# Optimization experiments

Hardware: AMD Instinct MI355X
Metric: run time of the kernel (lower is better)

## Reference

```python
import jax, jax.numpy as jnp
import numpy as np

B, G, N, D = 8, 16, 256, 768
E, S, SEQ = 1536, 128, 512
EPS = 1e-05


def rope_gn(x):
    # x: [b, g, n, h, s]; positions run over flattened (g, n), matching rope(x, dim=[1,2])
    g, n, half = x.shape[1], x.shape[2], x.shape[-1] // 2
    position = jnp.arange(g * n, dtype=jnp.float32).reshape(g, n)[:, :, None]  # [g,n,1]
    inv_freq = 10000.0 ** (jnp.arange(half, dtype=jnp.float32) / half)
    sinusoid = position[..., None] * inv_freq  # [g,n,1,half]
    sin, cos = jnp.sin(sinusoid), jnp.cos(sinusoid)
    x1, x2 = jnp.split(x, 2, axis=-1)
    return jnp.concatenate([x1 * cos - x2 * sin, x2 * cos + x1 * sin], axis=-1)


def rel_pos_bias(w, seq_len):
    # Toeplitz construction (seq_len <= 512 branch). w: [2*seq_len-1] -> [1, seq_len, seq_len]
    t = jnp.pad(w, (0, seq_len))                  # [3*seq_len-1]
    t = jnp.tile(t, seq_len)[:-seq_len]           # [seq_len*(3*seq_len-2)]
    t = t.reshape(seq_len, 3 * seq_len - 2)
    r = seq_len - 1                                # (2*seq_len-1)//2
    return t[:, r:-r][None]                        # [1, seq_len, seq_len]


def setup_inputs():
    key = jax.random.key(0)
    ks = jax.random.split(key, 8)
    inputs = jax.random.normal(ks[0], (B, G, N, D), dtype=jnp.float32)
    seg = jax.random.randint(ks[1], (B, G * N), 0, 4)
    segment_ids = jnp.sort(seg, axis=-1).reshape(B, G, N)
    params = {
        'ln_w': jnp.ones((D,), jnp.float32),
        'ln_b': jnp.zeros((D,), jnp.float32),
        'W1': jax.random.normal(ks[2], (D, 2 * E + S), jnp.float32) * 0.02,
        'b1': jnp.zeros((2 * E + S,), jnp.float32),
        'gamma': jax.random.uniform(ks[3], (4, S), jnp.float32),
        'beta': jax.random.uniform(ks[4], (4, S), jnp.float32),
        'W2': jax.random.normal(ks[5], (E, D), jnp.float32) * 0.02,
        'b2': jnp.zeros((D,), jnp.float32),
        'w_rel': jax.random.uniform(ks[6], (2 * SEQ - 1,), jnp.float32),
    }
    return dict(inputs=inputs, segment_ids=segment_ids, **params)


def reference(inputs, segment_ids, ln_w, ln_b, W1, b1, gamma, beta, W2, b2, w_rel):
    b, g, n, d = inputs.shape
    shortcut = inputs
    # LayerNorm
    mu = inputs.mean(-1, keepdims=True)
    var = ((inputs - mu) ** 2).mean(-1, keepdims=True)
    x = (inputs - mu) * jax.lax.rsqrt(var + EPS) * ln_w + ln_b
    # dense1 + silu, split into u, v, z
    uv = jax.nn.silu(x @ W1 + b1)
    u, v, z = uv[..., :E], uv[..., E:2 * E], uv[..., 2 * E:]
    # per-head affine gating + rope
    z = z[..., None, :] * gamma + beta            # [b,g,n,4,s]
    z = rope_gn(z)
    quad_q, quad_k, lin_q, lin_k = (z[..., i, :] for i in range(4))
    # non-causal global linear attention
    kv = jnp.einsum('bgcs,bgce->bse', lin_k, v)
    lin_v = jnp.einsum('bgcs,bse->bgce', lin_q, kv)
    lin_kv = jnp.einsum('bgnk,bgne->bgke', lin_k, lin_v) / n
    # segment mask over chunks
    mn = segment_ids.min(-1)
    mx = segment_ids.max(-1)
    mask = ((mn[:, :, None] <= mx[:, None, :]) & (mx[:, :, None] >= mn[:, None, :])).astype(inputs.dtype)
    mask = mask / mask.sum(-1, keepdims=True)
    lin_kv = jnp.einsum('bhke,bgh->bgke', lin_kv, mask)
    linear = jnp.einsum('bgnk,bgke->bgne', lin_q, lin_kv)
    # quadratic relu^2 attention with relative position bias
    qk = jnp.einsum('bgnk,bgmk->bgnm', quad_q, quad_k)
    bias = rel_pos_bias(w_rel, SEQ)[:, :n, :n]    # [1,n,n] broadcasts to [b,g,n,n]
    kernel = jnp.square(jax.nn.relu(qk / n + bias))
    quadratic = jnp.einsum('bgnm,bgme->bgne', kernel, v)
    out = (u * (quadratic + linear)) @ W2 + b2 + shortcut
    return out
```

## Files before the change

kernel.cpp:

```cpp
#include <hip/hip_runtime.h>
#include <math.h>

typedef __bf16 bf16;
typedef __bf16 bf16x8 __attribute__((ext_vector_type(8)));
typedef __bf16 bf16x4 __attribute__((ext_vector_type(4)));
typedef float  f32x4  __attribute__((ext_vector_type(4)));

#define D_   768
#define E_   1536
#define S_   128
#define TT_  32768
#define B_   8

#define OFF_W1T   0UL
#define OFF_W2T   4915200UL
#define OFF_TAB   7274496UL
#define OFF_XN    9375744UL
#define OFF_KER   OFF_XN
#define OFF_QQ    (OFF_XN + 16777216UL)
#define OFF_QK    (OFF_XN + 25165824UL)
#define OFF_LQ    (OFF_XN + 33554432UL)
#define OFF_U     59707392UL
#define OFF_Z     160370688UL
#define OFF_LK    168759296UL
#define OFF_LQT   177147904UL
#define OFF_LKT   185536512UL
#define OFF_MASK  193925120UL
#define OFF_INVF  193933312UL

__device__ __forceinline__ void gl_lds16(const bf16* g, bf16* l) {
  __builtin_amdgcn_global_load_lds(
      (const __attribute__((address_space(1))) unsigned int*)g,
      (__attribute__((address_space(3))) unsigned int*)l, 16, 0, 0);
}


#define STG(GB, LD, KT, DSTH) do {                                        \
  const int cg_ = (lane & 7) ^ ((lane >> 3) & 7);                         \
  const int rg_ = wave * 16 + ((lane >> 3) << 1) + (cg_ >> 2);            \
  gl_lds16((GB) + (long)rg_ * (LD) + (KT) * 32 + (cg_ & 3) * 8,           \
           (DSTH) + wave * 512);                                          \
} while (0)

template <class Epi, bool SWZ>
__global__ __launch_bounds__(512, 2) void gemm8p(
    const bf16* __restrict__ A, const bf16* __restrict__ B,
    int lda, int ldb, int K, Epi epi)
{
  __shared__ bf16 smem[4][4][4096];

  int bx = blockIdx.x, by = blockIdx.y;
  if constexpr (SWZ) {
    const int nbx = gridDim.x, nby = gridDim.y, nwg = nbx * nby;
    int bid = by * nbx + bx;
    const int q = nwg >> 3, r = nwg & 7;
    const int xcd = bid & 7, lid = bid >> 3;
    bid = (xcd < r ? xcd * (q + 1) : r * (q + 1) + (xcd - r) * q) + lid;
    const int gm = 8;
    const int pig = gm * nby;
    const int grp = bid / pig;
    const int fm = grp * gm;
    const int szm = min(nbx - fm, gm);
    const int loc = bid - grp * pig;
    bx = fm + loc % szm;
    by = loc / szm;
  }

  const int tid  = threadIdx.x;
  const int lane = tid & 63, wave = tid >> 6;
  const int wr = wave >> 2, wc = wave & 3;
  const int lrow = lane & 15, quad = lane >> 4;
  const int rb16 = (wc & 1) * 4;
  const int lbase = (lrow >> 1) * 128 +
                    (((((lrow & 1) << 2) | quad) ^ ((lrow >> 1) & 7)) * 16);

  const bf16* gA0 = A + (long)(bx * 256)       * lda;
  const bf16* gA1 = A + (long)(bx * 256 + 128) * lda;
  const bf16* gB0 = B + (long)(by * 256)       * ldb;
  const bf16* gB1 = B + (long)(by * 256 + 128) * ldb;

  f32x4 acc[8][4] = {};
  bf16x8 a0[4], a1[4], bfrag[4];

  const int NT = K >> 5;

#pragma unroll
  for (int t = 0; t < 3; ++t) {
    STG(gA0, lda, t, &smem[t][0][0]);
    STG(gA1, lda, t, &smem[t][1][0]);
    STG(gB0, ldb, t, &smem[t][2][0]);
    STG(gB1, ldb, t, &smem[t][3][0]);
  }
  asm volatile("s_waitcnt vmcnt(8)" ::: "memory");
  __builtin_amdgcn_s_barrier();
  __builtin_amdgcn_sched_barrier(0);

  for (int t = 0; t < NT; ++t) {
    const int st = t & 3, sp = (t + 3) & 3;
    const bf16* aBuf = &smem[st][wr][0];
    const bf16* bBuf = &smem[st][2 + (wc >> 1)][0];

#pragma unroll
    for (int mi = 0; mi < 4; ++mi)
      a0[mi] = *(const bf16x8*)((const char*)aBuf + mi * 1024 + lbase);
#pragma unroll
    for (int k = 0; k < 4; ++k)
      bfrag[k] = *(const bf16x8*)((const char*)bBuf + (rb16 + k) * 1024 + lbase);
#pragma unroll
    for (int mi = 0; mi < 4; ++mi)
      a1[mi] = *(const bf16x8*)((const char*)aBuf + (4 + mi) * 1024 + lbase);
    if (t + 3 < NT) {
      STG(gA0, lda, t + 3, &smem[sp][0][0]);
      STG(gB0, ldb, t + 3, &smem[sp][2][0]);
      STG(gA1, lda, t + 3, &smem[sp][1][0]);
      STG(gB1, ldb, t + 3, &smem[sp][3][0]);
    }

    __builtin_amdgcn_s_setprio(1);
#pragma unroll
    for (int mi = 0; mi < 4; ++mi)
#pragma unroll
      for (int n4 = 0; n4 < 4; ++n4)
        acc[mi][n4] = __builtin_amdgcn_mfma_f32_16x16x32_bf16(
            a0[mi], bfrag[n4], acc[mi][n4], 0, 0, 0);
#pragma unroll
    for (int mi = 0; mi < 4; ++mi)
#pragma unroll
      for (int n4 = 0; n4 < 4; ++n4)
        acc[4 + mi][n4] = __builtin_amdgcn_mfma_f32_16x16x32_bf16(
            a1[mi], bfrag[n4], acc[4 + mi][n4], 0, 0, 0);
    __builtin_amdgcn_s_setprio(0);

    __builtin_amdgcn_sched_barrier(0);
    if (t + 3 < NT)      asm volatile("s_waitcnt vmcnt(8)" ::: "memory");
    else if (t + 2 < NT) asm volatile("s_waitcnt vmcnt(4)" ::: "memory");
    else if (t + 1 < NT) asm volatile("s_waitcnt vmcnt(0)" ::: "memory");
    if (t + 1 < NT) {
      __builtin_amdgcn_s_barrier();
      __builtin_amdgcn_sched_barrier(0);
    }
  }

  const int rowbase = bx * 256 + wr * 128 + quad * 4;
  const int colbase = by * 256 + wc * 64 + lrow;
#pragma unroll
  for (int mi = 0; mi < 8; mi++)
#pragma unroll
    for (int ni = 0; ni < 4; ni++)
      epi(rowbase + mi * 16, colbase + ni * 16, 0, 0, acc[mi][ni]);
}

#define BM 128
#define BN 128
#define BK 32

template <class Epi, bool DUAL, bool SWZ = false>
__global__ __launch_bounds__(256) void gemm_bt(
    const bf16* __restrict__ A, const bf16* __restrict__ B,
    int lda, int ldb, int K,
    long sAb, long sAg, long sBb, long sBg,
    const bf16* __restrict__ A2, const bf16* __restrict__ B2,
    int lda2, int ldb2, int K2,
    long sA2b, long sA2g, long sB2b, long sB2g,
    int gdiv, Epi epi)
{
  __shared__ bf16 As[BM * BK];
  __shared__ bf16 Bs[BN * BK];
  const int z = blockIdx.z;
  const int bb = z / gdiv, gg = z % gdiv;

  int bx = blockIdx.x, by = blockIdx.y;
  if constexpr (SWZ) {
    const int nbx = gridDim.x, nby = gridDim.y, nwg = nbx * nby;
    int bid = by * nbx + bx;
    const int q = nwg >> 3, r = nwg & 7;
    const int xcd = bid & 7, lid = bid >> 3;
    bid = (xcd < r ? xcd * (q + 1) : r * (q + 1) + (xcd - r) * q) + lid;
    const int gm = 8;
    const int pig = gm * nby;
    const int grp = bid / pig;
    const int fm = grp * gm;
    const int szm = min(nbx - fm, gm);
    const int loc = bid - grp * pig;
    bx = fm + loc % szm;
    by = loc / szm;
  }

  const int tid  = threadIdx.x;
  const int lane = tid & 63, wave = tid >> 6;
  const int wm = (wave >> 1) * 64, wn = (wave & 1) * 64;
  const int lrow = lane & 15, quad = lane >> 4;
  const int srow = wave * 16 + (lane >> 2);
  const int scol = (lane & 3) * 8;
  bf16* ldsA0 = As + wave * 512;
  bf16* ldsA1 = As + (wave + 4) * 512;
  bf16* ldsB0 = Bs + wave * 512;
  bf16* ldsB1 = Bs + (wave + 4) * 512;

  f32x4 acc[4][4] = {};

  auto kloop = [&](const bf16* __restrict__ Ab, const bf16* __restrict__ Bb,
                   int lda_, int ldb_, int K_) {
    for (int k0 = 0; k0 < K_; k0 += BK) {
      __syncthreads();
      gl_lds16(Ab + (long)srow * lda_ + k0 + scol,        ldsA0);
      gl_lds16(Ab + (long)(srow + 64) * lda_ + k0 + scol, ldsA1);
      gl_lds16(Bb + (long)srow * ldb_ + k0 + scol,        ldsB0);
      gl_lds16(Bb + (long)(srow + 64) * ldb_ + k0 + scol, ldsB1);
      __syncthreads();
      bf16x8 af[4], bfr[4];
#pragma unroll
      for (int i = 0; i < 4; i++) af[i]  = *(const bf16x8*)&As[(wm + i * 16 + lrow) * BK + quad * 8];
#pragma unroll
      for (int i = 0; i < 4; i++) bfr[i] = *(const bf16x8*)&Bs[(wn + i * 16 + lrow) * BK + quad * 8];
#pragma unroll
      for (int mi = 0; mi < 4; mi++)
#pragma unroll
        for (int ni = 0; ni < 4; ni++)
          acc[mi][ni] = __builtin_amdgcn_mfma_f32_16x16x32_bf16(af[mi], bfr[ni], acc[mi][ni], 0, 0, 0);
    }
  };

  kloop(A + (long)bb * sAb + (long)gg * sAg + (long)bx * BM * lda,
        B + (long)bb * sBb + (long)gg * sBg + (long)by * BN * ldb, lda, ldb, K);
  if constexpr (DUAL)
    kloop(A2 + (long)bb * sA2b + (long)gg * sA2g + (long)bx * BM * lda2,
          B2 + (long)bb * sB2b + (long)gg * sB2g + (long)by * BN * ldb2, lda2, ldb2, K2);

  const int rowbase = bx * BM + wm + quad * 4;
  const int colbase = by * BN + wn + lrow;
#pragma unroll
  for (int mi = 0; mi < 4; mi++)
#pragma unroll
    for (int ni = 0; ni < 4; ni++)
      epi(rowbase + mi * 16, colbase + ni * 16, bb, gg, acc[mi][ni]);
}

struct EpiGemm1 {
  const float* b1; bf16* u; bf16* vT; bf16* z;
  __device__ void operator()(int row0, int col, int, int, f32x4 a) const {
    float s[4];
    const float bias = b1[col];
#pragma unroll
    for (int j = 0; j < 4; j++) {
      float x = a[j] + bias;
      float e = __expf(-x);
      s[j] = __fdividef(x, 1.f + e);
    }
    if (col < E_) {
#pragma unroll
      for (int j = 0; j < 4; j++) u[(long)(row0 + j) * E_ + col] = (bf16)s[j];
    } else if (col < 2 * E_) {
      const int e = col - E_, b = row0 >> 12, t = row0 & 4095;
      bf16x4 o;
#pragma unroll
      for (int j = 0; j < 4; j++) o[j] = (bf16)s[j];
      *(bf16x4*)&vT[((long)(b * E_ + e)) * 4096 + t] = o;
    } else {
      const int sc = col - 2 * E_;
#pragma unroll
      for (int j = 0; j < 4; j++) z[(long)(row0 + j) * S_ + sc] = (bf16)s[j];
    }
  }
};
struct EpiZ {
  const float* b1; bf16* z;
  __device__ void operator()(int row0, int col, int, int, f32x4 a) const {
    const float bias = b1[2 * E_ + col];
#pragma unroll
    for (int j = 0; j < 4; j++) {
      float x = a[j] + bias;
      float e = __expf(-x);
      z[(long)(row0 + j) * S_ + col] = (bf16)__fdividef(x, 1.f + e);
    }
  }
};
struct EpiF32 {
  float* C; long sCb, sCg; int ldc;
  __device__ void operator()(int row0, int col, int bb, int gg, f32x4 a) const {
#pragma unroll
    for (int j = 0; j < 4; j++)
      C[(long)bb * sCb + (long)gg * sCg + (long)(row0 + j) * ldc + col] = a[j];
  }
};
struct EpiBf16 {
  bf16* C; long sCb, sCg; int ldc;
  __device__ void operator()(int row0, int col, int bb, int gg, f32x4 a) const {
#pragma unroll
    for (int j = 0; j < 4; j++)
      C[(long)bb * sCb + (long)gg * sCg + (long)(row0 + j) * ldc + col] = (bf16)a[j];
  }
};
struct EpiKer {
  bf16* C; const float* wrel;
  __device__ void operator()(int row0, int col, int bb, int, f32x4 a) const {
#pragma unroll
    for (int j = 0; j < 4; j++) {
      float v = a[j] * (1.f / 256.f) + wrel[511 + col - (row0 + j)];
      v = fmaxf(v, 0.f);
      C[(long)bb * 65536 + (long)(row0 + j) * 256 + col] = (bf16)(v * v);
    }
  }
};
struct EpiCombine {
  bf16* u;
  __device__ void operator()(int row0, int col, int bb, int gg, f32x4 a) const {
#pragma unroll
    for (int j = 0; j < 4; j++) {
      long idx = ((long)((bb * 16 + gg) * 256 + row0 + j)) * E_ + col;
      u[idx] = (bf16)((float)u[idx] * a[j]);
    }
  }
};
struct EpiFinal {
  float* out; const float* b2; const float* x0;
  __device__ void operator()(int row0, int col, int, int, f32x4 a) const {
#pragma unroll
    for (int j = 0; j < 4; j++) {
      long idx = (long)(row0 + j) * D_ + col;
      out[idx] = a[j] + b2[col] + x0[idx];
    }
  }
};

__global__ __launch_bounds__(256) void ln_kernel(
    const float* __restrict__ x, const float* __restrict__ w,
    const float* __restrict__ b, bf16* __restrict__ xn)
{
  const long t = blockIdx.x;
  const float* row = x + t * D_;
  const int tid = threadIdx.x;
  float v0 = row[tid], v1 = row[tid + 256], v2 = row[tid + 512];
  float s = v0 + v1 + v2;
  float sq = v0 * v0 + v1 * v1 + v2 * v2;
#pragma unroll
  for (int off = 32; off; off >>= 1) {
    s  += __shfl_down(s, off, 64);
    sq += __shfl_down(sq, off, 64);
  }
  __shared__ float red[2][4];
  const int wave = tid >> 6, lane = tid & 63;
  if (lane == 0) { red[0][wave] = s; red[1][wave] = sq; }
  __syncthreads();
  s  = red[0][0] + red[0][1] + red[0][2] + red[0][3];
  sq = red[1][0] + red[1][1] + red[1][2] + red[1][3];
  const float mean = s * (1.f / 768.f);
  const float var  = sq * (1.f / 768.f) - mean * mean;
  const float rs   = rsqrtf(var + 1e-5f);
  xn[t * D_ + tid]       = (bf16)((v0 - mean) * rs * w[tid] + b[tid]);
  xn[t * D_ + tid + 256] = (bf16)((v1 - mean) * rs * w[tid + 256] + b[tid + 256]);
  xn[t * D_ + tid + 512] = (bf16)((v2 - mean) * rs * w[tid + 512] + b[tid + 512]);
}

template <class TI>
__global__ __launch_bounds__(256) void transpose_cast(
    const TI* __restrict__ in, bf16* __restrict__ out,
    int R, int C, long sInB, long sOutB)
{
  __shared__ float tile[64][65];
  const TI* ib = in  + (long)blockIdx.z * sInB;
  bf16*     ob = out + (long)blockIdx.z * sOutB;
  const int c0 = blockIdx.x * 64, r0 = blockIdx.y * 64;
  const int lc = threadIdx.x & 63, lr0 = threadIdx.x >> 6;
#pragma unroll
  for (int i = 0; i < 16; i++) {
    int r = lr0 + i * 4;
    tile[r][lc] = (float)ib[(long)(r0 + r) * C + c0 + lc];
  }
  __syncthreads();
#pragma unroll
  for (int i = 0; i < 16; i++) {
    int r = lr0 + i * 4;
    ob[(long)(c0 + r) * R + r0 + lc] = (bf16)tile[lc][r];
  }
}

__global__ __launch_bounds__(256) void rope_table_kernel(
    const float* __restrict__ invf, float2* __restrict__ tab)
{
  int idx = blockIdx.x * 256 + threadIdx.x;
  int p = idx >> 6, i = idx & 63;
  float arg = (float)p * invf[i];
  double a = (double)arg;
  tab[idx] = make_float2((float)sin(a), (float)cos(a));
}

__global__ __launch_bounds__(128) void rope_kernel(
    const bf16* __restrict__ zbuf, const float* __restrict__ gamma,
    const float* __restrict__ beta, const float2* __restrict__ tab,
    bf16* __restrict__ qq, bf16* __restrict__ qk,
    bf16* __restrict__ lq, bf16* __restrict__ lk)
{
  const long t = blockIdx.x;
  const int s = threadIdx.x;
  const int p = (int)(t & 4095);
  const int i = s & 63;
  const float2 sc = tab[p * 64 + i];
  const bf16* zr = zbuf + t * S_;
  const float zlo = (float)zr[i], zhi = (float)zr[i + 64];
  bf16* outs[4] = {qq, qk, lq, lk};
#pragma unroll
  for (int r = 0; r < 4; r++) {
    float zl = zlo * gamma[r * 128 + i]      + beta[r * 128 + i];
    float zh = zhi * gamma[r * 128 + i + 64] + beta[r * 128 + i + 64];
    float val = (s < 64) ? (zl * sc.y - zh * sc.x) : (zh * sc.y + zl * sc.x);
    outs[r][t * S_ + s] = (bf16)val;
  }
}

__global__ __launch_bounds__(64) void mask_kernel(const int* __restrict__ seg, float* __restrict__ mask) {
  __shared__ int mn[16], mx[16];
  const int b = blockIdx.x, tid = threadIdx.x;
  if (tid < 16) {
    const int* p = seg + (long)b * 4096 + tid * 256;
    int lo = p[0], hi = p[0];
    for (int i = 1; i < 256; i++) { int v = p[i]; lo = min(lo, v); hi = max(hi, v); }
    mn[tid] = lo; mx[tid] = hi;
  }
  __syncthreads();
  if (tid < 16) {
    const int g = tid;
    float row[16]; float s = 0.f;
    for (int h = 0; h < 16; h++) {
      float o = (mn[g] <= mx[h] && mx[g] >= mn[h]) ? 1.f : 0.f;
      row[h] = o; s += o;
    }
    const float inv = 1.f / s;
    for (int h = 0; h < 16; h++) mask[((long)b * 16 + g) * 16 + h] = row[h] * inv;
  }
}

__global__ __launch_bounds__(256) void mix_kernel(
    const float* __restrict__ P2, const float* __restrict__ mask, bf16* __restrict__ amix)
{
  const int z = blockIdx.x;
  const int b = z >> 4;
  float m[16];
#pragma unroll
  for (int h = 0; h < 16; h++) m[h] = mask[(long)z * 16 + h] * (1.f / 256.f);
  const float* Pb = P2 + (long)b * 16 * 16384;
  bf16* Ab = amix + (long)z * 16384;
#pragma unroll 4
  for (int j = 0; j < 16; j++) {
    int c = j * 256 + threadIdx.x;
    float ax = 0, ay = 0, az = 0, aw = 0;
#pragma unroll
    for (int h = 0; h < 16; h++) {
      float4 p = ((const float4*)(Pb + (long)h * 16384))[c];
      ax += m[h] * p.x; ay += m[h] * p.y; az += m[h] * p.z; aw += m[h] * p.w;
    }
    bf16x4 o; o[0] = (bf16)ax; o[1] = (bf16)ay; o[2] = (bf16)az; o[3] = (bf16)aw;
    *(bf16x4*)&Ab[(long)c * 4] = o;
  }
}

extern "C" void kernel_launch(void* const* d_in, const int* in_sizes, int n_in,
                              void* d_out, int out_size, void* d_ws, size_t ws_size,
                              hipStream_t stream)
{
  const float* x0    = (const float*)d_in[0];
  const int*   seg   = (const int*)d_in[1];
  const float* lnw   = (const float*)d_in[2];
  const float* lnb   = (const float*)d_in[3];
  const float* W1    = (const float*)d_in[4];
  const float* b1    = (const float*)d_in[5];
  const float* gamma = (const float*)d_in[6];
  const float* beta  = (const float*)d_in[7];
  const float* W2    = (const float*)d_in[8];
  const float* b2    = (const float*)d_in[9];
  const float* wrel  = (const float*)d_in[10];
  float* out = (float*)d_out;
  char* ws = (char*)d_ws;

  bf16*   w1t   = (bf16*)(ws + OFF_W1T);
  bf16*   w2t   = (bf16*)(ws + OFF_W2T);
  float2* tab   = (float2*)(ws + OFF_TAB);
  bf16*   xn    = (bf16*)(ws + OFF_XN);
  bf16*   ker   = (bf16*)(ws + OFF_KER);
  bf16*   qq    = (bf16*)(ws + OFF_QQ);
  bf16*   qk    = (bf16*)(ws + OFF_QK);
  bf16*   lq    = (bf16*)(ws + OFF_LQ);
  bf16*   u     = (bf16*)(ws + OFF_U);
  bf16*   zb    = (bf16*)(ws + OFF_Z);
  float*  P2    = (float*)(ws + OFF_Z);
  bf16*   lk    = (bf16*)(ws + OFF_LK);
  bf16*   T1    = (bf16*)(ws + OFF_LK);
  bf16*   lqT   = (bf16*)(ws + OFF_LQT);
  bf16*   amix  = (bf16*)(ws + OFF_LQT);
  bf16*   kvT   = (bf16*)(ws + OFF_LQT + 4194304UL);
  bf16*   lkT   = (bf16*)(ws + OFF_LKT);
  float*  maskb = (float*)(ws + OFF_MASK);
  float*  invfd = (float*)(ws + OFF_INVF);
  bf16*   vTd   = (bf16*)d_out;

  static float h_invf[64];
  for (int i = 0; i < 64; i++) h_invf[i] = powf(10000.0f, (float)i * (1.0f / 64.0f));
  hipMemcpyAsync(invfd, h_invf, 64 * sizeof(float), hipMemcpyHostToDevice, stream);

  transpose_cast<float><<<dim3(50, 12, 1), 256, 0, stream>>>(W1, w1t, 768, 3200, 0, 0);
  transpose_cast<float><<<dim3(12, 24, 1), 256, 0, stream>>>(W2, w2t, 1536, 768, 0, 0);
  rope_table_kernel<<<1024, 256, 0, stream>>>(invfd, tab);
  mask_kernel<<<8, 64, 0, stream>>>(seg, maskb);

  ln_kernel<<<TT_, 256, 0, stream>>>(x0, lnw, lnb, xn);

  gemm8p<EpiGemm1, true><<<dim3(128, 12), 512, 0, stream>>>(
      xn, w1t, 768, 768, 768, EpiGemm1{b1, u, vTd, zb});
  gemm_bt<EpiZ, false><<<dim3(256, 1, 1), 256, 0, stream>>>(
      xn, w1t + (long)3072 * 768, 768, 768, 768, 0, 0, 0, 0,
      nullptr, nullptr, 0, 0, 0, 0, 0, 0, 0, 1, EpiZ{b1, zb});

  rope_kernel<<<TT_, 128, 0, stream>>>(zb, gamma, beta, tab, qq, qk, lq, lk);

  transpose_cast<bf16><<<dim3(2, 64, 8), 256, 0, stream>>>(lq, lqT, 4096, 128, 524288, 524288);
  transpose_cast<bf16><<<dim3(2, 64, 8), 256, 0, stream>>>(lk, lkT, 4096, 128, 524288, 524288);

  gemm_bt<EpiF32, false><<<dim3(1, 1, 128), 256, 0, stream>>>(
      lqT, lkT, 4096, 4096, 256, 524288, 256, 524288, 256,
      nullptr, nullptr, 0, 0, 0, 0, 0, 0, 0, 16, EpiF32{P2, 262144, 16384, 128});

  mix_kernel<<<128, 256, 0, stream>>>(P2, maskb, amix);

  gemm_bt<EpiBf16, false><<<dim3(12, 1, 8), 256, 0, stream>>>(
      vTd, lkT, 4096, 4096, 4096, 6291456, 0, 524288, 0,
      nullptr, nullptr, 0, 0, 0, 0, 0, 0, 0, 1, EpiBf16{kvT, 196608, 0, 128});

  gemm_bt<EpiBf16, false><<<dim3(2, 1, 128), 256, 0, stream>>>(
      lq, amix, 128, 128, 128, 32768, 0, 16384, 0,
      nullptr, nullptr, 0, 0, 0, 0, 0, 0, 0, 1, EpiBf16{T1, 32768, 0, 128});

  gemm_bt<EpiKer, false><<<dim3(2, 2, 128), 256, 0, stream>>>(
      qq, qk, 128, 128, 128, 32768, 0, 32768, 0,
      nullptr, nullptr, 0, 0, 0, 0, 0, 0, 0, 1, EpiKer{ker, wrel});

  gemm_bt<EpiCombine, true><<<dim3(2, 12, 128), 256, 0, stream>>>(
      ker, vTd, 256, 4096, 256, 1048576, 65536, 6291456, 256,
      T1, kvT, 128, 128, 128, 524288, 32768, 196608, 0, 16, EpiCombine{u});

  gemm8p<EpiFinal, true><<<dim3(128, 3), 512, 0, stream>>>(
      u, w2t, 1536, 1536, 1536, EpiFinal{out, b2, x0});
}
```

Measured before the change: 972.5 us.

## Replace 256x256 8-wave GEMM with 128x128 4-wave triple-buffered GEMM

The two large projection GEMMs now use a 256-thread kernel with 128x128 output tiles, a 3-stage LDS ring instead of 4 stages, and two 16-byte global-to-LDS loads per lane per operand. The grids double in each dimension. For the final GEMM this raises the workgroup count from 384 to 1536, which should fill the GPU's CUs better, and the smaller LDS footprint allows three blocks per CU. In exchange each tile reuses loaded data less and the prefetch depth is shallower.

```diff
diff --git a/kernel.cpp b/kernel.cpp
--- a/kernel.cpp
+++ b/kernel.cpp
@@ -35,19 +35,21 @@
 }
 
 
-#define STG(GB, LD, KT, DSTH) do {                                        \
+#define STG2(GB, LD, KT, DSTH) do {                                       \
   const int cg_ = (lane & 7) ^ ((lane >> 3) & 7);                         \
-  const int rg_ = wave * 16 + ((lane >> 3) << 1) + (cg_ >> 2);            \
+  const int rg_ = wave * 32 + ((lane >> 3) << 1) + (cg_ >> 2);            \
   gl_lds16((GB) + (long)rg_ * (LD) + (KT) * 32 + (cg_ & 3) * 8,           \
-           (DSTH) + wave * 512);                                          \
+           (DSTH) + wave * 1024);                                         \
+  gl_lds16((GB) + (long)(rg_ + 16) * (LD) + (KT) * 32 + (cg_ & 3) * 8,    \
+           (DSTH) + wave * 1024 + 512);                                   \
 } while (0)
 
 template <class Epi, bool SWZ>
-__global__ __launch_bounds__(512, 2) void gemm8p(
+__global__ __launch_bounds__(256, 3) void gemm3s(
     const bf16* __restrict__ A, const bf16* __restrict__ B,
     int lda, int ldb, int K, Epi epi)
 {
-  __shared__ bf16 smem[4][4][4096];
+  __shared__ bf16 smem[3][2][4096];
 
   int bx = blockIdx.x, by = blockIdx.y;
   if constexpr (SWZ) {
@@ -68,83 +70,67 @@
 
   const int tid  = threadIdx.x;
   const int lane = tid & 63, wave = tid >> 6;
-  const int wr = wave >> 2, wc = wave & 3;
+  const int wr = wave >> 1, wc = wave & 1;
   const int lrow = lane & 15, quad = lane >> 4;
-  const int rb16 = (wc & 1) * 4;
   const int lbase = (lrow >> 1) * 128 +
                     (((((lrow & 1) << 2) | quad) ^ ((lrow >> 1) & 7)) * 16);
 
-  const bf16* gA0 = A + (long)(bx * 256)       * lda;
-  const bf16* gA1 = A + (long)(bx * 256 + 128) * lda;
-  const bf16* gB0 = B + (long)(by * 256)       * ldb;
-  const bf16* gB1 = B + (long)(by * 256 + 128) * ldb;
-
-  f32x4 acc[8][4] = {};
-  bf16x8 a0[4], a1[4], bfrag[4];
+  const bf16* gA = A + (long)(bx * 128) * lda;
+  const bf16* gB = B + (long)(by * 128) * ldb;
+
+  f32x4 acc[4][4] = {};
+  bf16x8 af[4], bf_[4];
 
   const int NT = K >> 5;
 
-#pragma unroll
-  for (int t = 0; t < 3; ++t) {
-    STG(gA0, lda, t, &smem[t][0][0]);
-    STG(gA1, lda, t, &smem[t][1][0]);
-    STG(gB0, ldb, t, &smem[t][2][0]);
-    STG(gB1, ldb, t, &smem[t][3][0]);
-  }
-  asm volatile("s_waitcnt vmcnt(8)" ::: "memory");
+  STG2(gA, lda, 0, &smem[0][0][0]);
+  STG2(gB, ldb, 0, &smem[0][1][0]);
+  STG2(gA, lda, 1, &smem[1][0][0]);
+  STG2(gB, ldb, 1, &smem[1][1][0]);
+  asm volatile("s_waitcnt vmcnt(4)" ::: "memory");
   __builtin_amdgcn_s_barrier();
   __builtin_amdgcn_sched_barrier(0);
 
+  int st = 0, sp = 2;
   for (int t = 0; t < NT; ++t) {
-    const int st = t & 3, sp = (t + 3) & 3;
-    const bf16* aBuf = &smem[st][wr][0];
-    const bf16* bBuf = &smem[st][2 + (wc >> 1)][0];
+    const bf16* aBuf = &smem[st][0][0];
+    const bf16* bBuf = &smem[st][1][0];
 
 #pragma unroll
     for (int mi = 0; mi < 4; ++mi)
-      a0[mi] = *(const bf16x8*)((const char*)aBuf + mi * 1024 + lbase);
-#pragma unroll
-    for (int k = 0; k < 4; ++k)
-      bfrag[k] = *(const bf16x8*)((const char*)bBuf + (rb16 + k) * 1024 + lbase);
+      af[mi] = *(const bf16x8*)((const char*)aBuf + (wr * 4 + mi) * 1024 + lbase);
+#pragma unroll
+    for (int ni = 0; ni < 4; ++ni)
+      bf_[ni] = *(const bf16x8*)((const char*)bBuf + (wc * 4 + ni) * 1024 + lbase);
+    if (t + 2 < NT) {
+      STG2(gA, lda, t + 2, &smem[sp][0][0]);
+      STG2(gB, ldb, t + 2, &smem[sp][1][0]);
+    }
+
+    __builtin_amdgcn_s_setprio(1);
 #pragma unroll
     for (int mi = 0; mi < 4; ++mi)
-      a1[mi] = *(const bf16x8*)((const char*)aBuf + (4 + mi) * 1024 + lbase);
-    if (t + 3 < NT) {
-      STG(gA0, lda, t + 3, &smem[sp][0][0]);
-      STG(gB0, ldb, t + 3, &smem[sp][2][0]);
-      STG(gA1, lda, t + 3, &smem[sp][1][0]);
-      STG(gB1, ldb, t + 3, &smem[sp][3][0]);
-    }
-
-    __builtin_amdgcn_s_setprio(1);
-#pragma unroll
-    for (int mi = 0; mi < 4; ++mi)
-#pragma unroll
-      for (int n4 = 0; n4 < 4; ++n4)
-        acc[mi][n4] = __builtin_amdgcn_mfma_f32_16x16x32_bf16(
-            a0[mi], bfrag[n4], acc[mi][n4], 0, 0, 0);
-#pragma unroll
-    for (int mi = 0; mi < 4; ++mi)
-#pragma unroll
-      for (int n4 = 0; n4 < 4; ++n4)
-        acc[4 + mi][n4] = __builtin_amdgcn_mfma_f32_16x16x32_bf16(
-            a1[mi], bfrag[n4], acc[4 + mi][n4], 0, 0, 0);
+#pragma unroll
+      for (int ni = 0; ni < 4; ++ni)
+        acc[mi][ni] = __builtin_amdgcn_mfma_f32_16x16x32_bf16(
+            af[mi], bf_[ni], acc[mi][ni], 0, 0, 0);
     __builtin_amdgcn_s_setprio(0);
 
     __builtin_amdgcn_sched_barrier(0);
-    if (t + 3 < NT)      asm volatile("s_waitcnt vmcnt(8)" ::: "memory");
-    else if (t + 2 < NT) asm volatile("s_waitcnt vmcnt(4)" ::: "memory");
+    if (t + 2 < NT)      asm volatile("s_waitcnt vmcnt(4)" ::: "memory");
     else if (t + 1 < NT) asm volatile("s_waitcnt vmcnt(0)" ::: "memory");
     if (t + 1 < NT) {
       __builtin_amdgcn_s_barrier();
       __builtin_amdgcn_sched_barrier(0);
     }
-  }
-
-  const int rowbase = bx * 256 + wr * 128 + quad * 4;
-  const int colbase = by * 256 + wc * 64 + lrow;
-#pragma unroll
-  for (int mi = 0; mi < 8; mi++)
+    st = (st == 2) ? 0 : st + 1;
+    sp = (sp == 2) ? 0 : sp + 1;
+  }
+
+  const int rowbase = bx * 128 + wr * 64 + quad * 4;
+  const int colbase = by * 128 + wc * 64 + lrow;
+#pragma unroll
+  for (int mi = 0; mi < 4; mi++)
 #pragma unroll
     for (int ni = 0; ni < 4; ni++)
       epi(rowbase + mi * 16, colbase + ni * 16, 0, 0, acc[mi][ni]);
@@ -504,7 +490,7 @@
 
   ln_kernel<<<TT_, 256, 0, stream>>>(x0, lnw, lnb, xn);
 
-  gemm8p<EpiGemm1, true><<<dim3(128, 12), 512, 0, stream>>>(
+  gemm3s<EpiGemm1, true><<<dim3(256, 24), 256, 0, stream>>>(
       xn, w1t, 768, 768, 768, EpiGemm1{b1, u, vTd, zb});
   gemm_bt<EpiZ, false><<<dim3(256, 1, 1), 256, 0, stream>>>(
       xn, w1t + (long)3072 * 768, 768, 768, 768, 0, 0, 0, 0,
@@ -537,6 +523,6 @@
       ker, vTd, 256, 4096, 256, 1048576, 65536, 6291456, 256,
       T1, kvT, 128, 128, 128, 524288, 32768, 196608, 0, 16, EpiCombine{u});
 
-  gemm8p<EpiFinal, true><<<dim3(128, 3), 512, 0, stream>>>(
+  gemm3s<EpiFinal, true><<<dim3(256, 6), 256, 0, stream>>>(
       u, w2t, 1536, 1536, 1536, EpiFinal{out, b2, x0});
 }
```

Measured after the change: 942.6 us. 1.03x faster.
